# Performance work log

Hardware: AMD Instinct MI355X
Metric: run time of the kernel (lower is better)

The kernel has to match this reference:

```python
import jax, jax.numpy as jnp
import numpy as np

L = 2048      # max_length / encoder sequence length
E = 1024      # eo_hidden_size
H = 1024      # hidden_size
D = 512       # embed_size
V = 32000     # vocab_size
MV = 32768    # max_vocab_size


def setup_inputs() -> dict:
    key = jax.random.key(0)
    ks = jax.random.split(key, 20)
    s = 0.02
    return {
        "inp": jax.random.randint(ks[0], (1,), 0, V),
        "hidden": jax.random.normal(ks[1], (1, 1, H), jnp.float32),
        "encoder_outputs": jax.random.normal(ks[2], (L, E), jnp.float32),
        "input_seq": jax.random.randint(ks[3], (L,), 0, MV),
        "pre_prob": jax.random.randint(ks[4], (L,), 0, 2),
        "emb": jax.random.normal(ks[5], (V, D), jnp.float32) * s,
        "attn_W": jax.random.normal(ks[6], (L, H + D), jnp.float32) * s,
        "attn_b": jnp.zeros((L,), jnp.float32),
        "comb_W": jax.random.normal(ks[7], (H, E + D), jnp.float32) * s,
        "comb_b": jnp.zeros((H,), jnp.float32),
        "W_ih": jax.random.normal(ks[8], (3 * H, H + E), jnp.float32) * s,
        "W_hh": jax.random.normal(ks[9], (3 * H, H), jnp.float32) * s,
        "b_ih": jnp.zeros((3 * H,), jnp.float32),
        "b_hh": jnp.zeros((3 * H,), jnp.float32),
        "Wo_W": jax.random.normal(ks[10], (V, H), jnp.float32) * s,
        "Wo_b": jnp.zeros((V,), jnp.float32),
        "Wc_W": jax.random.normal(ks[11], (H, E), jnp.float32) * s,
        "Wc_b": jnp.zeros((H,), jnp.float32),
    }


def reference(inp, hidden, encoder_outputs, input_seq, pre_prob,
              emb, attn_W, attn_b, comb_W, comb_b,
              W_ih, W_hh, b_ih, b_hh, Wo_W, Wo_b, Wc_W, Wc_b):
    tok = inp[0]
    # --- copy-mechanism selective read (int path, matches torch .long() trunc) ---
    sel_w = (input_seq == tok).astype(jnp.int32) * pre_prob.astype(jnp.int32)  # [L]
    eo_int = jax.lax.stop_gradient(encoder_outputs).astype(jnp.int32)          # trunc toward 0
    sel_reading = (sel_w @ eo_int).astype(jnp.float32)                          # [E]
    # --- embedding (OOV -> UNK id 2); dropout is identity in eval ---
    embed_idx = jnp.where(tok >= V, 2, tok)
    embedded = emb[embed_idx]                                                   # [D]
    h = hidden[0, 0]                                                            # [H]
    # --- attention over encoder outputs ---
    attn_weights = jax.nn.softmax(attn_W @ jnp.concatenate([embedded, h]) + attn_b)  # [L]
    attn_applied = attn_weights @ encoder_outputs                               # [E]
    out = jax.nn.relu(comb_W @ jnp.concatenate([embedded, attn_applied]) + comb_b)   # [H]
    # --- single GRU step (torch gate order: r, z, n) ---
    x = jnp.concatenate([out, sel_reading])                                     # [H+E]
    gi = W_ih @ x + b_ih
    gh = W_hh @ h + b_hh
    r = jax.nn.sigmoid(gi[:H] + gh[:H])
    z = jax.nn.sigmoid(gi[H:2 * H] + gh[H:2 * H])
    n = jnp.tanh(gi[2 * H:] + r * gh[2 * H:])
    h_new = (1.0 - z) * n + z * h                                               # [H]
    # --- generate vs copy scores ---
    score_g = Wo_W @ h_new + Wo_b                                               # [V]
    score_c = jnp.tanh(encoder_outputs @ Wc_W.T + Wc_b) @ h_new                 # [L]
    score = jax.nn.softmax(jnp.concatenate([score_g, score_c]))                 # [V+L]
    prob_g, prob_c = score[:V], score[V:]
    # pad generate probs to MV and scatter-add copy probs (== mm with one-hot)
    out1 = jnp.zeros((MV,), score.dtype).at[:V].set(prob_g)
    out1 = out1.at[input_seq].add(prob_c)
    out1 = jnp.where(out1 == 0, 1e-9, out1)
    out1 = out1.at[2].set(1e-9)
    out1 = jnp.log(out1)
    return (out1[None, :], h_new[None, None, :], attn_weights[None, :], prob_c[None, :])
```

## Files before the change

### kernel.cpp

```cpp
#include <hip/hip_runtime.h>
#include <math.h>

#define LQ 2048
#define EQ 1024
#define HQ 1024
#define DQ 512
#define VQ 32000
#define MVQ 32768

#define OUT1_OFF 0
#define HNEW_OFF 32768
#define AW_OFF   33792
#define PC_OFF   35840

#define PSZ 2097152
#define KSPLIT 4

typedef __attribute__((ext_vector_type(8))) short short8_t;
typedef __attribute__((ext_vector_type(8))) unsigned short ushort8_t;
typedef __attribute__((ext_vector_type(4))) float floatx4;

__device__ inline float wred(float v) {
    v += __shfl_down(v, 32);
    v += __shfl_down(v, 16);
    v += __shfl_down(v, 8);
    v += __shfl_down(v, 4);
    v += __shfl_down(v, 2);
    v += __shfl_down(v, 1);
    return v;
}
__device__ inline float wred_max(float v) {
    v = fmaxf(v, __shfl_down(v, 32));
    v = fmaxf(v, __shfl_down(v, 16));
    v = fmaxf(v, __shfl_down(v, 8));
    v = fmaxf(v, __shfl_down(v, 4));
    v = fmaxf(v, __shfl_down(v, 2));
    v = fmaxf(v, __shfl_down(v, 1));
    return v;
}
__device__ inline float sigmoidf_(float x) { return 1.0f / (1.0f + expf(-x)); }
__device__ inline unsigned short f2bf(float x) {
    unsigned int u = __float_as_uint(x);
    unsigned int r = (u + 0x7fffu + ((u >> 16) & 1u)) >> 16;
    return (unsigned short)r;
}
__device__ inline float bf2f(unsigned short b) {
    return __uint_as_float(((unsigned int)b) << 16);
}
__device__ __forceinline__ void gload16(const unsigned short* g,
                                        unsigned short* l) {
    __builtin_amdgcn_global_load_lds(
        (const __attribute__((address_space(1))) unsigned int*)g,
        (__attribute__((address_space(3))) unsigned int*)l, 16, 0, 0);
}

__global__ __launch_bounds__(256) void k_prep(
    const float* __restrict__ enc, const float* __restrict__ Wc,
    const int* __restrict__ inp, const int* __restrict__ input_seq,
    const int* __restrict__ pre_prob,
    const float* __restrict__ attn_W, const float* __restrict__ attn_b,
    const float* __restrict__ emb, const float* __restrict__ hidden,
    unsigned short* __restrict__ Ah, unsigned short* __restrict__ Al,
    unsigned short* __restrict__ Bh, unsigned short* __restrict__ Bl,
    float* __restrict__ x2, float* __restrict__ logits, float* __restrict__ aa)
{
    __shared__ int s_cnt;
    __shared__ int s_list[LQ];
    const int tid = threadIdx.x;
    const int bx = blockIdx.x;
    if (bx < 512) {
        if (bx < 4) aa[bx * 256 + tid] = 0.0f;
        int warp = tid >> 6, lane = tid & 63;
        int r = bx * 4 + warp;
        int tok = inp[0];
        int ei = (tok >= VQ) ? 2 : tok;
        const float4* Wr = (const float4*)(attn_W + (size_t)r * 1536);
        const float4* e4 = (const float4*)(emb + (size_t)ei * DQ);
        const float4* h4 = (const float4*)hidden;
        float acc = 0.0f;
        #pragma unroll
        for (int i = 0; i < 6; ++i) {
            int idx = lane + i * 64;
            float4 x = (idx < 128) ? e4[idx] : h4[idx - 128];
            float4 w = Wr[idx];
            acc += w.x * x.x + w.y * x.y + w.z * x.z + w.w * x.w;
        }
        acc = wred(acc);
        if (lane == 0) logits[r] = acc + attn_b[r];
        return;
    }
    if (bx == 512) {
        if (tid == 0) s_cnt = 0;
        __syncthreads();
        int tok = inp[0];
        for (int l = tid; l < LQ; l += 256) {
            if (input_seq[l] == tok && pre_prob[l] != 0) {
                int p = atomicAdd(&s_cnt, 1);
                s_list[p] = l;
            }
        }
        __syncthreads();
        int nm = s_cnt;
        for (int e = tid; e < EQ; e += 256) {
            int acc = 0;
            for (int j = 0; j < nm; ++j)
                acc += (int)enc[(size_t)s_list[j] * EQ + e];
            x2[HQ + e] = (float)acc;
        }
        return;
    }
    size_t e0 = ((size_t)(bx - 513) * 256 + tid) * 8;
    const float* src;
    unsigned short *hdst, *ldst;
    size_t off;
    if (e0 < (size_t)LQ * EQ) { src = enc; hdst = Ah; ldst = Al; off = e0; }
    else { src = Wc; hdst = Bh; ldst = Bl; off = e0 - (size_t)LQ * EQ; }
    float4 v0 = *(const float4*)(src + off);
    float4 v1 = *(const float4*)(src + off + 4);
    float vv[8] = {v0.x, v0.y, v0.z, v0.w, v1.x, v1.y, v1.z, v1.w};
    ushort8_t H, L;
    #pragma unroll
    for (int k = 0; k < 8; ++k) {
        float x = vv[k];
        unsigned short hb = f2bf(x);
        H[k] = hb;
        L[k] = f2bf(x - bf2f(hb));
    }
    *(ushort8_t*)(hdst + off) = H;
    *(ushort8_t*)(ldst + off) = L;
}

__global__ __launch_bounds__(256, 2) void k_gemm_fused(
    const unsigned short* __restrict__ Ah, const unsigned short* __restrict__ Al,
    const unsigned short* __restrict__ Bh, const unsigned short* __restrict__ Bl,
    float* __restrict__ P,
    const float* __restrict__ logits, const float* __restrict__ enc,
    float* __restrict__ aa, float* __restrict__ aw_out,
    const float* __restrict__ W_ih, const float* __restrict__ W_hh,
    const float* __restrict__ comb_W, const int* __restrict__ inp,
    const float* __restrict__ emb, const float* __restrict__ hidden,
    const float* __restrict__ x2,
    float* __restrict__ gi_sel, float* __restrict__ gh_pre,
    float* __restrict__ pre_c)
{
    __shared__ unsigned short sm[2 * 4 * 4096];
    const int b = blockIdx.x, t = threadIdx.x;
    const int lane = t & 63, wid = t >> 6;

    if (b < 512) {
        const int n0 = (b & 7) * 128;
        const int m0 = ((b >> 3) & 15) * 128;
        const int zz = b >> 7;
        const int kz = zz * 256;
        float* Pz = P + (size_t)zz * PSZ;
        const unsigned short* tsrc =
            (wid == 0) ? Ah + (size_t)m0 * EQ :
            (wid == 1) ? Al + (size_t)m0 * EQ :
            (wid == 2) ? Bh + (size_t)n0 * EQ :
                         Bl + (size_t)n0 * EQ;
        const int srow = lane >> 2, schunk = lane & 3;
        const int wm = (wid >> 1) * 64, wn = (wid & 1) * 64;
        const int fr = lane & 15, kg = lane >> 4;

        floatx4 acc[4][4];
        #pragma unroll
        for (int i = 0; i < 4; ++i)
            #pragma unroll
            for (int j = 0; j < 4; ++j)
                acc[i][j] = (floatx4){0.f, 0.f, 0.f, 0.f};

        #define STAGE(buf, s)                                                  \
            {                                                                  \
                unsigned short* dst = sm + (buf) * 16384 + wid * 4096;         \
                _Pragma("unroll")                                              \
                for (int c = 0; c < 8; ++c) {                                  \
                    int row = c * 16 + srow;                                   \
                    int gch = schunk ^ ((row >> 1) & 3);                       \
                    gload16(tsrc + (size_t)row * EQ + kz + (s) * 32 + gch * 8, \
                            dst + c * 512);                                    \
                }                                                              \
            }

        STAGE(0, 0);
        __syncthreads();
        for (int s = 0; s < 8; ++s) {
            int cur = s & 1;
            if (s < 7) STAGE(cur ^ 1, s + 1);
            const char* base = (const char*)sm + cur * 32768;
            short8_t fah[4], fal[4], fbh[4], fbl[4];
            #pragma unroll
            for (int f = 0; f < 4; ++f) {
                int ra = wm + f * 16 + fr;
                int oa = ra * 64 + ((kg ^ ((ra >> 1) & 3)) * 16);
                fah[f] = *(const short8_t*)(base + oa);
                fal[f] = *(const short8_t*)(base + 8192 + oa);
                int rb = wn + f * 16 + fr;
                int ob = rb * 64 + ((kg ^ ((rb >> 1) & 3)) * 16);
                fbh[f] = *(const short8_t*)(base + 16384 + ob);
                fbl[f] = *(const short8_t*)(base + 24576 + ob);
            }
            #pragma unroll
            for (int i = 0; i < 4; ++i)
                #pragma unroll
                for (int j = 0; j < 4; ++j) {
                    acc[i][j] = __builtin_amdgcn_mfma_f32_16x16x32_bf16(
                        fah[i], fbh[j], acc[i][j], 0, 0, 0);
                    acc[i][j] = __builtin_amdgcn_mfma_f32_16x16x32_bf16(
                        fal[i], fbh[j], acc[i][j], 0, 0, 0);
                    acc[i][j] = __builtin_amdgcn_mfma_f32_16x16x32_bf16(
                        fah[i], fbl[j], acc[i][j], 0, 0, 0);
                }
            __syncthreads();
        }
        #pragma unroll
        for (int i = 0; i < 4; ++i)
            #pragma unroll
            for (int j = 0; j < 4; ++j) {
                int row = m0 + wm + i * 16 + kg * 4;
                int col = n0 + wn + j * 16 + fr;
                #pragma unroll
                for (int r = 0; r < 4; ++r)
                    Pz[(size_t)(row + r) * HQ + col] = acc[i][j][r];
            }
        return;
    }
    if (b < 576) {
        float* sred = (float*)sm;
        float* s_w  = (float*)sm + 8;
        int sb = b - 512;
        int xb = sb & 3, yb = sb >> 2;
        float m = -3.4e38f;
        for (int i = t; i < LQ; i += 256) m = fmaxf(m, logits[i]);
        m = wred_max(m);
        if (lane == 0) sred[wid] = m;
        __syncthreads();
        if (t == 0)
            sred[0] = fmaxf(fmaxf(sred[0], sred[1]), fmaxf(sred[2], sred[3]));
        __syncthreads();
        m = sred[0];
        __syncthreads();
        float s = 0.0f;
        for (int i = t; i < LQ; i += 256) s += expf(logits[i] - m);
        s = wred(s);
        if (lane == 0) sred[wid] = s;
        __syncthreads();
        if (t == 0) sred[0] = sred[0] + sred[1] + sred[2] + sred[3];
        __syncthreads();
        s = sred[0];
        int l0 = yb * 128;
        if (t < 128) {
            float w = expf(logits[l0 + t] - m) / s;
            s_w[t] = w;
            if (xb == 0) aw_out[l0 + t] = w;
        }
        __syncthreads();
        int e = xb * 256 + t;
        float acc = 0.0f;
        for (int l = 0; l < 128; ++l)
            acc = fmaf(s_w[l], enc[(size_t)(l0 + l) * EQ + e], acc);
        atomicAdd(&aa[e], acc);
        return;
    }
    if (b < 1344) {
        int row = (b - 576) * 4 + wid;
        const float4* Wr = (const float4*)(W_ih + (size_t)row * 2048 + 1024);
        const float4* xs = (const float4*)(x2 + HQ);
        float acc = 0.0f;
        #pragma unroll
        for (int c = 0; c < 4; ++c) {
            int idx = lane + c * 64;
            float4 w = Wr[idx], x = xs[idx];
            acc += w.x * x.x + w.y * x.y + w.z * x.z + w.w * x.w;
        }
        acc = wred(acc);
        if (lane == 0) gi_sel[row] = acc;
        return;
    }
    if (b < 2112) {
        int row = (b - 1344) * 4 + wid;
        const float4* Wr = (const float4*)(W_hh + (size_t)row * 1024);
        const float4* hv = (const float4*)hidden;
        float acc = 0.0f;
        #pragma unroll
        for (int c = 0; c < 4; ++c) {
            int idx = lane + c * 64;
            float4 w = Wr[idx], x = hv[idx];
            acc += w.x * x.x + w.y * x.y + w.z * x.z + w.w * x.w;
        }
        acc = wred(acc);
        if (lane == 0) gh_pre[row] = acc;
        return;
    }
    {
        int row = (b - 2112) * 4 + wid;
        int tok = inp[0];
        int ei = (tok >= VQ) ? 2 : tok;
        const float4* Wr = (const float4*)(comb_W + (size_t)row * 1536);
        const float4* e4 = (const float4*)(emb + (size_t)ei * DQ);
        float acc = 0.0f;
        #pragma unroll
        for (int c = 0; c < 2; ++c) {
            int idx = lane + c * 64;
            float4 w = Wr[idx], x = e4[idx];
            acc += w.x * x.x + w.y * x.y + w.z * x.z + w.w * x.w;
        }
        acc = wred(acc);
        if (lane == 0) pre_c[row] = acc;
        return;
    }
}

__global__ __launch_bounds__(256) void k_comb(
    const float* __restrict__ W, const float* __restrict__ b,
    const float* __restrict__ pre_c, const float* __restrict__ aa,
    float* __restrict__ x2)
{
    int warp = threadIdx.x >> 6, lane = threadIdx.x & 63;
    int r = blockIdx.x * 4 + warp;
    const float4* Wr = (const float4*)(W + (size_t)r * 1536 + 512);
    const float4* a4 = (const float4*)aa;
    float acc = 0.0f;
    #pragma unroll
    for (int i = 0; i < 4; ++i) {
        int idx = lane + i * 64;
        float4 w = Wr[idx], x = a4[idx];
        acc += w.x * x.x + w.y * x.y + w.z * x.z + w.w * x.w;
    }
    acc = wred(acc);
    if (lane == 0) x2[r] = fmaxf(acc + pre_c[r] + b[r], 0.0f);
}

__global__ __launch_bounds__(256) void k_gru(
    const float* __restrict__ W_ih, const float* __restrict__ gi_sel,
    const float* __restrict__ gh_pre,
    const float* __restrict__ b_ih, const float* __restrict__ b_hh,
    const float* __restrict__ x2, const float* __restrict__ h,
    float* __restrict__ hnew, float* __restrict__ out_h)
{
    int warp = threadIdx.x >> 6, lane = threadIdx.x & 63;
    int i = blockIdx.x * 4 + warp;
    const float4* xv = (const float4*)x2;
    const float4* Wr = (const float4*)(W_ih + (size_t)i * 2048);
    const float4* Wz = (const float4*)(W_ih + (size_t)(HQ + i) * 2048);
    const float4* Wn = (const float4*)(W_ih + (size_t)(2 * HQ + i) * 2048);
    float ar = 0, az = 0, an = 0;
    #pragma unroll
    for (int c = 0; c < 4; ++c) {
        int idx = lane + c * 64;
        float4 x = xv[idx];
        float4 w = Wr[idx]; ar += w.x*x.x + w.y*x.y + w.z*x.z + w.w*x.w;
        w = Wz[idx];        az += w.x*x.x + w.y*x.y + w.z*x.z + w.w*x.w;
        w = Wn[idx];        an += w.x*x.x + w.y*x.y + w.z*x.z + w.w*x.w;
    }
    ar = wred(ar); az = wred(az); an = wred(an);
    if (lane == 0) {
        float gir = ar + gi_sel[i] + b_ih[i];
        float giz = az + gi_sel[HQ + i] + b_ih[HQ + i];
        float gin = an + gi_sel[2 * HQ + i] + b_ih[2 * HQ + i];
        float ghr = gh_pre[i] + b_hh[i];
        float ghz = gh_pre[HQ + i] + b_hh[HQ + i];
        float ghn = gh_pre[2 * HQ + i] + b_hh[2 * HQ + i];
        float r = sigmoidf_(gir + ghr);
        float z = sigmoidf_(giz + ghz);
        float n = tanhf(gin + r * ghn);
        float hn = (1.0f - z) * n + z * h[i];
        hnew[i] = hn;
        out_h[i] = hn;
    }
}

__global__ __launch_bounds__(256) void k_scores(
    const float* __restrict__ Wo_W, const float* __restrict__ Wo_b,
    const float* __restrict__ P, const float* __restrict__ Wc_b,
    const float* __restrict__ hnew, float* __restrict__ score)
{
    int warp = threadIdx.x >> 6, lane = threadIdx.x & 63;
    int r = blockIdx.x * 4 + warp;
    const float4* hv = (const float4*)hnew;
    float acc = 0.0f;
    if (r < VQ) {
        const float4* Wr = (const float4*)(Wo_W + (size_t)r * HQ);
        #pragma unroll
        for (int i = 0; i < 4; ++i) {
            int idx = lane + i * 64;
            float4 w = Wr[idx], x = hv[idx];
            acc += w.x * x.x + w.y * x.y + w.z * x.z + w.w * x.w;
        }
        acc = wred(acc);
        if (lane == 0) score[r] = acc + Wo_b[r];
    } else {
        int l = r - VQ;
        const float4* P0 = (const float4*)(P + (size_t)l * HQ);
        const float4* P1 = (const float4*)(P + (size_t)PSZ + (size_t)l * HQ);
        const float4* P2 = (const float4*)(P + 2 * (size_t)PSZ + (size_t)l * HQ);
        const float4* P3 = (const float4*)(P + 3 * (size_t)PSZ + (size_t)l * HQ);
        #pragma unroll
        for (int i = 0; i < 4; ++i) {
            int idx = lane + i * 64;
            float4 a = P0[idx], b1 = P1[idx], b2 = P2[idx], b3 = P3[idx];
            float4 bb = *(const float4*)(Wc_b + idx * 4);
            float4 x = hv[idx];
            acc += tanhf(a.x + b1.x + b2.x + b3.x + bb.x) * x.x +
                   tanhf(a.y + b1.y + b2.y + b3.y + bb.y) * x.y +
                   tanhf(a.z + b1.z + b2.z + b3.z + bb.z) * x.z +
                   tanhf(a.w + b1.w + b2.w + b3.w + bb.w) * x.w;
        }
        acc = wred(acc);
        if (lane == 0) score[VQ + l] = acc;
    }
}

__global__ __launch_bounds__(256) void k_final(
    const float* __restrict__ score, const int* __restrict__ input_seq,
    float* __restrict__ out1, float* __restrict__ out_pc)
{
    __shared__ float sred[4];
    __shared__ float bins[256];
    const int N = VQ + LQ;
    int tid = threadIdx.x, wid = tid >> 6, lane = tid & 63;
    float m = -3.4e38f;
    for (int i = tid; i < N; i += 256) m = fmaxf(m, score[i]);
    m = wred_max(m);
    if (lane == 0) sred[wid] = m;
    __syncthreads();
    if (tid == 0)
        sred[0] = fmaxf(fmaxf(sred[0], sred[1]), fmaxf(sred[2], sred[3]));
    __syncthreads();
    m = sred[0];
    __syncthreads();
    float s = 0.0f;
    for (int i = tid; i < N; i += 256) s += expf(score[i] - m);
    s = wred(s);
    if (lane == 0) sred[wid] = s;
    __syncthreads();
    if (tid == 0) sred[0] = sred[0] + sred[1] + sred[2] + sred[3];
    __syncthreads();
    s = sred[0];
    bins[tid] = 0.0f;
    __syncthreads();
    int i0 = blockIdx.x * 256;
    for (int l = tid; l < LQ; l += 256) {
        int si = input_seq[l];
        if (si >= i0 && si < i0 + 256)
            atomicAdd(&bins[si - i0], expf(score[VQ + l] - m) / s);
    }
    if (blockIdx.x < 8) {
        int l = blockIdx.x * 256 + tid;
        out_pc[l] = expf(score[VQ + l] - m) / s;
    }
    __syncthreads();
    int i = i0 + tid;
    float v = ((i < VQ) ? expf(score[i] - m) / s : 0.0f) + bins[tid];
    if (i == 2 || v == 0.0f) v = 1e-9f;
    out1[i] = logf(v);
}

extern "C" void kernel_launch(void* const* d_in, const int* in_sizes, int n_in,
                              void* d_out, int out_size, void* d_ws, size_t ws_size,
                              hipStream_t stream) {
    const int*   inp       = (const int*)  d_in[0];
    const float* hidden    = (const float*)d_in[1];
    const float* enc       = (const float*)d_in[2];
    const int*   input_seq = (const int*)  d_in[3];
    const int*   pre_prob  = (const int*)  d_in[4];
    const float* emb       = (const float*)d_in[5];
    const float* attn_W    = (const float*)d_in[6];
    const float* attn_b    = (const float*)d_in[7];
    const float* comb_W    = (const float*)d_in[8];
    const float* comb_b    = (const float*)d_in[9];
    const float* W_ih      = (const float*)d_in[10];
    const float* W_hh      = (const float*)d_in[11];
    const float* b_ih      = (const float*)d_in[12];
    const float* b_hh      = (const float*)d_in[13];
    const float* Wo_W      = (const float*)d_in[14];
    const float* Wo_b      = (const float*)d_in[15];
    const float* Wc_W      = (const float*)d_in[16];
    const float* Wc_b      = (const float*)d_in[17];

    float* out = (float*)d_out;

    unsigned short* Ah = (unsigned short*)d_ws;
    unsigned short* Al = Ah + (size_t)LQ * EQ;
    unsigned short* Bh = Al + (size_t)LQ * EQ;
    unsigned short* Bl = Bh + (size_t)HQ * EQ;
    float* P      = (float*)(Bl + (size_t)HQ * EQ);
    float* x2     = P + (size_t)KSPLIT * PSZ;
    float* hnew   = x2 + 2048;
    float* logits = hnew + 1024;
    float* aa     = logits + 2048;
    float* score  = aa + 1024;
    float* gi_sel = score + 34048;
    float* gh_pre = gi_sel + 3072;
    float* pre_c  = gh_pre + 3072;

    k_prep<<<2049, 256, 0, stream>>>(enc, Wc_W, inp, input_seq, pre_prob,
                                     attn_W, attn_b, emb, hidden,
                                     Ah, Al, Bh, Bl, x2, logits, aa);
    k_gemm_fused<<<2368, 256, 0, stream>>>(Ah, Al, Bh, Bl, P, logits, enc,
                                           aa, out + AW_OFF, W_ih, W_hh,
                                           comb_W, inp, emb, hidden, x2,
                                           gi_sel, gh_pre, pre_c);
    k_comb<<<HQ / 4, 256, 0, stream>>>(comb_W, comb_b, pre_c, aa, x2);
    k_gru<<<HQ / 4, 256, 0, stream>>>(W_ih, gi_sel, gh_pre, b_ih, b_hh, x2,
                                      hidden, hnew, out + HNEW_OFF);
    k_scores<<<(VQ + LQ) / 4, 256, 0, stream>>>(Wo_W, Wo_b, P, Wc_b, hnew,
                                                score);
    k_final<<<MVQ / 256, 256, 0, stream>>>(score, input_seq, out + OUT1_OFF,
                                           out + PC_OFF);
}
```

Before: 120.5 us.

## Drop split-K in enc@Wc GEMM, fuse bias+tanh epilogue, simplify copy scores

The enc·Wcᵀ GEMM previously split K into 4 partial fp32 buffers (4×8MB) that k_scores summed before applying bias and tanh. Now each block computes the full K=1024 with 64×64 tiles and writes tanh(acc+bias) directly into one buffer. k_scores then treats those rows like the vocab rows. This cuts the partial-sum write and read traffic by about 4x, at the cost of smaller tiles with less reuse and a longer serial K loop per block. Occupancy is raised to 4 blocks per CU.

Measured after the change: 112.5 us. 1.07x faster.

```diff
diff --git a/kernel.cpp b/kernel.cpp
--- a/kernel.cpp
+++ b/kernel.cpp
@@ -12,9 +12,6 @@
 #define HNEW_OFF 32768
 #define AW_OFF   33792
 #define PC_OFF   35840
-
-#define PSZ 2097152
-#define KSPLIT 4
 
 typedef __attribute__((ext_vector_type(8))) short short8_t;
 typedef __attribute__((ext_vector_type(8))) unsigned short ushort8_t;
@@ -130,10 +127,10 @@
     *(ushort8_t*)(ldst + off) = L;
 }
 
-__global__ __launch_bounds__(256, 2) void k_gemm_fused(
+__global__ __launch_bounds__(256, 4) void k_gemm_fused(
     const unsigned short* __restrict__ Ah, const unsigned short* __restrict__ Al,
     const unsigned short* __restrict__ Bh, const unsigned short* __restrict__ Bl,
-    float* __restrict__ P,
+    float* __restrict__ T, const float* __restrict__ Wc_b,
     const float* __restrict__ logits, const float* __restrict__ enc,
     float* __restrict__ aa, float* __restrict__ aw_out,
     const float* __restrict__ W_ih, const float* __restrict__ W_hh,
@@ -143,66 +140,63 @@
     float* __restrict__ gi_sel, float* __restrict__ gh_pre,
     float* __restrict__ pre_c)
 {
-    __shared__ unsigned short sm[2 * 4 * 4096];
+    __shared__ unsigned short sm[2 * 4 * 2048];
     const int b = blockIdx.x, t = threadIdx.x;
     const int lane = t & 63, wid = t >> 6;
 
     if (b < 512) {
-        const int n0 = (b & 7) * 128;
-        const int m0 = ((b >> 3) & 15) * 128;
-        const int zz = b >> 7;
-        const int kz = zz * 256;
-        float* Pz = P + (size_t)zz * PSZ;
+        const int n0 = (b & 15) * 64;
+        const int m0 = (b >> 4) * 64;
         const unsigned short* tsrc =
             (wid == 0) ? Ah + (size_t)m0 * EQ :
             (wid == 1) ? Al + (size_t)m0 * EQ :
             (wid == 2) ? Bh + (size_t)n0 * EQ :
                          Bl + (size_t)n0 * EQ;
         const int srow = lane >> 2, schunk = lane & 3;
-        const int wm = (wid >> 1) * 64, wn = (wid & 1) * 64;
+        const int wm = (wid >> 1) * 32, wn = (wid & 1) * 32;
         const int fr = lane & 15, kg = lane >> 4;
 
-        floatx4 acc[4][4];
-        #pragma unroll
-        for (int i = 0; i < 4; ++i)
+        floatx4 acc[2][2];
+        #pragma unroll
+        for (int i = 0; i < 2; ++i)
             #pragma unroll
-            for (int j = 0; j < 4; ++j)
+            for (int j = 0; j < 2; ++j)
                 acc[i][j] = (floatx4){0.f, 0.f, 0.f, 0.f};
 
         #define STAGE(buf, s)                                                  \
             {                                                                  \
-                unsigned short* dst = sm + (buf) * 16384 + wid * 4096;         \
+                unsigned short* dst = sm + (buf) * 8192 + wid * 2048;          \
                 _Pragma("unroll")                                              \
-                for (int c = 0; c < 8; ++c) {                                  \
+                for (int c = 0; c < 4; ++c) {                                  \
                     int row = c * 16 + srow;                                   \
                     int gch = schunk ^ ((row >> 1) & 3);                       \
-                    gload16(tsrc + (size_t)row * EQ + kz + (s) * 32 + gch * 8, \
+                    gload16(tsrc + (size_t)row * EQ + (s) * 32 + gch * 8,      \
                             dst + c * 512);                                    \
                 }                                                              \
             }
 
         STAGE(0, 0);
         __syncthreads();
-        for (int s = 0; s < 8; ++s) {
+        for (int s = 0; s < 32; ++s) {
             int cur = s & 1;
-            if (s < 7) STAGE(cur ^ 1, s + 1);
-            const char* base = (const char*)sm + cur * 32768;
-            short8_t fah[4], fal[4], fbh[4], fbl[4];
+            if (s < 31) STAGE(cur ^ 1, s + 1);
+            const char* base = (const char*)sm + cur * 16384;
+            short8_t fah[2], fal[2], fbh[2], fbl[2];
             #pragma unroll
-            for (int f = 0; f < 4; ++f) {
+            for (int f = 0; f < 2; ++f) {
                 int ra = wm + f * 16 + fr;
                 int oa = ra * 64 + ((kg ^ ((ra >> 1) & 3)) * 16);
                 fah[f] = *(const short8_t*)(base + oa);
-                fal[f] = *(const short8_t*)(base + 8192 + oa);
+                fal[f] = *(const short8_t*)(base + 4096 + oa);
                 int rb = wn + f * 16 + fr;
                 int ob = rb * 64 + ((kg ^ ((rb >> 1) & 3)) * 16);
-                fbh[f] = *(const short8_t*)(base + 16384 + ob);
-                fbl[f] = *(const short8_t*)(base + 24576 + ob);
+                fbh[f] = *(const short8_t*)(base + 8192 + ob);
+                fbl[f] = *(const short8_t*)(base + 12288 + ob);
             }
             #pragma unroll
-            for (int i = 0; i < 4; ++i)
+            for (int i = 0; i < 2; ++i)
                 #pragma unroll
-                for (int j = 0; j < 4; ++j) {
+                for (int j = 0; j < 2; ++j) {
                     acc[i][j] = __builtin_amdgcn_mfma_f32_16x16x32_bf16(
                         fah[i], fbh[j], acc[i][j], 0, 0, 0);
                     acc[i][j] = __builtin_amdgcn_mfma_f32_16x16x32_bf16(
@@ -213,14 +207,15 @@
             __syncthreads();
         }
         #pragma unroll
-        for (int i = 0; i < 4; ++i)
+        for (int i = 0; i < 2; ++i)
             #pragma unroll
-            for (int j = 0; j < 4; ++j) {
+            for (int j = 0; j < 2; ++j) {
                 int row = m0 + wm + i * 16 + kg * 4;
                 int col = n0 + wn + j * 16 + fr;
+                float bj = Wc_b[col];
                 #pragma unroll
                 for (int r = 0; r < 4; ++r)
-                    Pz[(size_t)(row + r) * HQ + col] = acc[i][j][r];
+                    T[(size_t)(row + r) * HQ + col] = tanhf(acc[i][j][r] + bj);
             }
         return;
     }
@@ -371,43 +366,24 @@
 
 __global__ __launch_bounds__(256) void k_scores(
     const float* __restrict__ Wo_W, const float* __restrict__ Wo_b,
-    const float* __restrict__ P, const float* __restrict__ Wc_b,
-    const float* __restrict__ hnew, float* __restrict__ score)
+    const float* __restrict__ T, const float* __restrict__ hnew,
+    float* __restrict__ score)
 {
     int warp = threadIdx.x >> 6, lane = threadIdx.x & 63;
     int r = blockIdx.x * 4 + warp;
     const float4* hv = (const float4*)hnew;
+    const float* Wr = (r < VQ) ? Wo_W + (size_t)r * HQ
+                               : T + (size_t)(r - VQ) * HQ;
+    const float4* W4 = (const float4*)Wr;
     float acc = 0.0f;
-    if (r < VQ) {
-        const float4* Wr = (const float4*)(Wo_W + (size_t)r * HQ);
-        #pragma unroll
-        for (int i = 0; i < 4; ++i) {
-            int idx = lane + i * 64;
-            float4 w = Wr[idx], x = hv[idx];
-            acc += w.x * x.x + w.y * x.y + w.z * x.z + w.w * x.w;
-        }
-        acc = wred(acc);
-        if (lane == 0) score[r] = acc + Wo_b[r];
-    } else {
-        int l = r - VQ;
-        const float4* P0 = (const float4*)(P + (size_t)l * HQ);
-        const float4* P1 = (const float4*)(P + (size_t)PSZ + (size_t)l * HQ);
-        const float4* P2 = (const float4*)(P + 2 * (size_t)PSZ + (size_t)l * HQ);
-        const float4* P3 = (const float4*)(P + 3 * (size_t)PSZ + (size_t)l * HQ);
-        #pragma unroll
-        for (int i = 0; i < 4; ++i) {
-            int idx = lane + i * 64;
-            float4 a = P0[idx], b1 = P1[idx], b2 = P2[idx], b3 = P3[idx];
-            float4 bb = *(const float4*)(Wc_b + idx * 4);
-            float4 x = hv[idx];
-            acc += tanhf(a.x + b1.x + b2.x + b3.x + bb.x) * x.x +
-                   tanhf(a.y + b1.y + b2.y + b3.y + bb.y) * x.y +
-                   tanhf(a.z + b1.z + b2.z + b3.z + bb.z) * x.z +
-                   tanhf(a.w + b1.w + b2.w + b3.w + bb.w) * x.w;
-        }
-        acc = wred(acc);
-        if (lane == 0) score[VQ + l] = acc;
-    }
+    #pragma unroll
+    for (int i = 0; i < 4; ++i) {
+        int idx = lane + i * 64;
+        float4 w = W4[idx], x = hv[idx];
+        acc += w.x * x.x + w.y * x.y + w.z * x.z + w.w * x.w;
+    }
+    acc = wred(acc);
+    if (lane == 0) score[r] = acc + ((r < VQ) ? Wo_b[r] : 0.0f);
 }
 
 __global__ __launch_bounds__(256) void k_final(
@@ -483,8 +459,8 @@
     unsigned short* Al = Ah + (size_t)LQ * EQ;
     unsigned short* Bh = Al + (size_t)LQ * EQ;
     unsigned short* Bl = Bh + (size_t)HQ * EQ;
-    float* P      = (float*)(Bl + (size_t)HQ * EQ);
-    float* x2     = P + (size_t)KSPLIT * PSZ;
+    float* T      = (float*)(Bl + (size_t)HQ * EQ);
+    float* x2     = T + (size_t)LQ * HQ;
     float* hnew   = x2 + 2048;
     float* logits = hnew + 1024;
     float* aa     = logits + 2048;
@@ -496,15 +472,14 @@
     k_prep<<<2049, 256, 0, stream>>>(enc, Wc_W, inp, input_seq, pre_prob,
                                      attn_W, attn_b, emb, hidden,
                                      Ah, Al, Bh, Bl, x2, logits, aa);
-    k_gemm_fused<<<2368, 256, 0, stream>>>(Ah, Al, Bh, Bl, P, logits, enc,
-                                           aa, out + AW_OFF, W_ih, W_hh,
+    k_gemm_fused<<<2368, 256, 0, stream>>>(Ah, Al, Bh, Bl, T, Wc_b, logits,
+                                           enc, aa, out + AW_OFF, W_ih, W_hh,
                                            comb_W, inp, emb, hidden, x2,
                                            gi_sel, gh_pre, pre_c);
     k_comb<<<HQ / 4, 256, 0, stream>>>(comb_W, comb_b, pre_c, aa, x2);
     k_gru<<<HQ / 4, 256, 0, stream>>>(W_ih, gi_sel, gh_pre, b_ih, b_hh, x2,
                                       hidden, hnew, out + HNEW_OFF);
-    k_scores<<<(VQ + LQ) / 4, 256, 0, stream>>>(Wo_W, Wo_b, P, Wc_b, hnew,
-                                                score);
+    k_scores<<<(VQ + LQ) / 4, 256, 0, stream>>>(Wo_W, Wo_b, T, hnew, score);
     k_final<<<MVQ / 256, 256, 0, stream>>>(score, input_seq, out + OUT1_OFF,
                                            out + PC_OFF);
 }
```
